# Performance work log

Measured on AMD Instinct MI355X. Metric: run time of the kernel, lower is better.

## Reference

```python
import jax, jax.numpy as jnp
import numpy as np

B, C, H, W = 4, 256, 64, 64
C8 = C // 8

def setup_inputs() -> dict:
    key = jax.random.key(0)
    ks = jax.random.split(key, 9)
    s_in = 1.0 / np.sqrt(C)
    return {
        "feat1": jax.random.normal(ks[0], (B, C, H, W), jnp.float32),
        "feat2": jax.random.normal(ks[1], (B, C, H, W), jnp.float32),
        # 1x1 conv weights stored as [out_ch, in_ch]
        "Wq": jax.random.normal(ks[2], (C8, C), jnp.float32) * s_in,
        "bq": jax.random.normal(ks[3], (C8,), jnp.float32) * s_in,
        "Wk": jax.random.normal(ks[4], (C8, C), jnp.float32) * s_in,
        "bk": jax.random.normal(ks[5], (C8,), jnp.float32) * s_in,
        "Wv": jax.random.normal(ks[6], (C, C), jnp.float32) * s_in,
        "bv": jax.random.normal(ks[7], (C,), jnp.float32) * s_in,
        "gamma": jax.random.normal(ks[8], (1,), jnp.float32) * 0.1,
    }

def reference(feat1, feat2, Wq, bq, Wk, bk, Wv, bv, gamma):
    b, c, h, w = feat1.shape
    n = h * w
    f1 = feat1.reshape(b, c, n)  # [B,C,N]
    f2 = feat2.reshape(b, c, n)
    # 1x1 convs == per-pixel channel matmuls
    q = jnp.einsum("oc,bcn->bno", Wq, f1) + bq            # [B,N,C8]
    k = jnp.einsum("oc,bcn->bon", Wk, f2) + bk[None, :, None]  # [B,C8,N]
    v = jnp.einsum("oc,bcn->bon", Wv, f2) + bv[None, :, None]  # [B,C,N]
    energy = jnp.einsum("bno,bom->bnm", q, k)             # [B,N,N] (unscaled)
    attn = jax.nn.softmax(energy, axis=-1)
    # out[b,c,m] = sum_n v[b,c,n] * attn[b,m,n]
    out = jnp.einsum("bcn,bmn->bcm", v, attn).reshape(b, c, h, w)
    return gamma * out + feat1
```

## Files before the change

kernel.cpp:

```cpp
#include <hip/hip_runtime.h>
#include <hip/hip_bf16.h>
#include <stdint.h>

typedef __attribute__((ext_vector_type(8))) short bf16x8;
typedef __attribute__((ext_vector_type(4))) short short4v;
typedef __attribute__((ext_vector_type(4))) float f32x4;
typedef __attribute__((ext_vector_type(16))) float f32x16;
typedef __attribute__((ext_vector_type(4))) unsigned uint4v;

#define LDS3(p) ((__attribute__((address_space(3))) void*)(p))
#define GLB1(p) ((const __attribute__((address_space(1))) void*)(p))

constexpr int Bc = 4;
constexpr int Cc = 256;
constexpr int Nn = 4096;
constexpr int Dq = 32;
constexpr float L2E = 1.4426950408889634f;

__device__ __forceinline__ short f2b(float x) {
  union { float f; uint32_t u; } v; v.f = x;
  uint32_t r = (v.u + 0x7fffu + ((v.u >> 16) & 1u)) >> 16;
  return (short)(r & 0xffffu);
}
__device__ __forceinline__ float b2f(short s) {
  union { uint32_t u; float f; } v; v.u = ((uint32_t)(uint16_t)s) << 16;
  return v.f;
}
__device__ __forceinline__ unsigned fb(float x) {
  union { float f; unsigned u; } v; v.f = x; return v.u;
}

__global__ __launch_bounds__(256) void prep_transpose(
    const float* __restrict__ f1, const float* __restrict__ f2,
    short* __restrict__ f1T, short* __restrict__ f2T) {
  __shared__ float tile[64][65];
  const int bx = blockIdx.x;
  const int which = bx >> 10;
  const int rem = bx & 1023;
  const int b = rem >> 8;
  const int cb = (rem >> 6) & 3;
  const int nb = rem & 63;
  const float* src = which ? f2 : f1;
  short* dst = which ? f2T : f1T;
  const int c0 = cb * 64, n0 = nb * 64;
  const int tid = threadIdx.x;
  const int lane = tid & 63;
  const int row4 = tid >> 6;
#pragma unroll
  for (int i = 0; i < 16; ++i) {
    const int cl = row4 + i * 4;
    tile[cl][lane] = src[(size_t)(b * Cc + c0 + cl) * Nn + n0 + lane];
  }
  __syncthreads();
#pragma unroll
  for (int i = 0; i < 16; ++i) {
    const int nl = row4 + i * 4;
    dst[(size_t)(b * Nn + n0 + nl) * Cc + c0 + lane] = f2b(tile[lane][nl]);
  }
}

__global__ __launch_bounds__(256) void prep_weights(
    const float* __restrict__ Wq, const float* __restrict__ Wk,
    const float* __restrict__ Wv, short* __restrict__ Wq_b,
    short* __restrict__ Wk_b, short* __restrict__ Wv_b) {
  const int base = (blockIdx.x * 256 + threadIdx.x) * 4;
#pragma unroll
  for (int j = 0; j < 4; ++j) {
    const int idx = base + j;
    if (idx < 8192) Wq_b[idx] = f2b(Wq[idx]);
    else if (idx < 16384) Wk_b[idx - 8192] = f2b(Wk[idx - 8192]);
    else if (idx < 16384 + 65536) Wv_b[idx - 16384] = f2b(Wv[idx - 16384]);
  }
}

__global__ __launch_bounds__(256) void proj_qkv(
    const short* __restrict__ f1T, const short* __restrict__ f2T,
    const short* __restrict__ Wq_b, const float* __restrict__ bq,
    const short* __restrict__ Wk_b, const float* __restrict__ bk,
    const short* __restrict__ Wv_b, const float* __restrict__ bv,
    short* __restrict__ q_ws, short* __restrict__ k_ws,
    short* __restrict__ v_ws) {
  const int bx = blockIdx.x;
  const int b = bx >> 6;
  const int n0 = (bx & 63) * 64;
  const int tid = threadIdx.x;
  const int w = tid >> 6;
  const int lane = tid & 63;
  const int l16 = lane & 15;
  const int g = lane >> 4;

#pragma unroll
  for (int qk = 0; qk < 2; ++qk) {
    const short* X = qk ? f2T : f1T;
    const short* Wm = qk ? Wk_b : Wq_b;
    const float* bias_p = qk ? bk : bq;
    short* outp = qk ? k_ws : q_ws;
    f32x4 accq[2] = {(f32x4){0.f, 0.f, 0.f, 0.f}, (f32x4){0.f, 0.f, 0.f, 0.f}};
#pragma unroll
    for (int kc = 0; kc < 8; ++kc) {
      const bf16x8 a = *(const bf16x8*)&X[(size_t)(b * Nn + n0 + w * 16 + l16) * Cc + kc * 32 + g * 8];
#pragma unroll
      for (int ob = 0; ob < 2; ++ob) {
        const bf16x8 bb = *(const bf16x8*)&Wm[(ob * 16 + l16) * Cc + kc * 32 + g * 8];
        accq[ob] = __builtin_amdgcn_mfma_f32_16x16x32_bf16(a, bb, accq[ob], 0, 0, 0);
      }
    }
#pragma unroll
    for (int ob = 0; ob < 2; ++ob) {
      const float bias = bias_p[ob * 16 + l16];
#pragma unroll
      for (int r = 0; r < 4; ++r) {
        const int n = n0 + w * 16 + g * 4 + r;
        outp[(size_t)(b * Nn + n) * Dq + ob * 16 + l16] = f2b(accq[ob][r] + bias);
      }
    }
  }

  {
    f32x4 acc[4][4];
#pragma unroll
    for (int ci = 0; ci < 4; ++ci)
#pragma unroll
      for (int nb = 0; nb < 4; ++nb) acc[ci][nb] = (f32x4){0.f, 0.f, 0.f, 0.f};
#pragma unroll
    for (int kc = 0; kc < 8; ++kc) {
      bf16x8 bfr[4];
#pragma unroll
      for (int nb = 0; nb < 4; ++nb)
        bfr[nb] = *(const bf16x8*)&f2T[(size_t)(b * Nn + n0 + nb * 16 + l16) * Cc + kc * 32 + g * 8];
#pragma unroll
      for (int ci = 0; ci < 4; ++ci) {
        const bf16x8 afr = *(const bf16x8*)&Wv_b[((w * 4 + ci) * 16 + l16) * Cc + kc * 32 + g * 8];
#pragma unroll
        for (int nb = 0; nb < 4; ++nb)
          acc[ci][nb] = __builtin_amdgcn_mfma_f32_16x16x32_bf16(afr, bfr[nb], acc[ci][nb], 0, 0, 0);
      }
    }
#pragma unroll
    for (int ci = 0; ci < 4; ++ci) {
#pragma unroll
      for (int r = 0; r < 4; ++r) {
        const int c = (w * 4 + ci) * 16 + g * 4 + r;
        const float bias = bv[c];
#pragma unroll
        for (int nb = 0; nb < 4; ++nb) {
          const int n = n0 + nb * 16 + l16;
          v_ws[(size_t)(b * Cc + c) * Nn + n] = f2b(acc[ci][nb][r] + bias);
        }
      }
    }
  }
}

constexpr int NT = 32;
constexpr int VBUF = 256 * NT * 2;
constexpr int SBYTES = 2 * VBUF;

template <int KS>
__global__ __launch_bounds__(256, 2) void attn_kernel(
    const short* __restrict__ q_ws, const short* __restrict__ k_ws,
    const short* __restrict__ v_ws, short* __restrict__ Opart,
    float* __restrict__ mlm, short* __restrict__ mll) {
  constexpr int KSPAN = Nn / KS;
  constexpr int NTILES = KSPAN / NT;
  __shared__ __align__(16) char smem[SBYTES];
  const int bx = blockIdx.x;
  const int swz = (bx & 7) * (16 * KS) + (bx >> 3);
  const int ks = swz >> 7;
  const int rem = swz & 127;
  const int b = rem >> 5;
  const int m0 = (rem & 31) * 128;
  const int n0 = ks * KSPAN;
  const int tid = threadIdx.x;
  const int w = tid >> 6;
  const int lane = tid & 63;
  const int l31 = lane & 31;
  const int h = lane >> 5;

  const short* qbase = q_ws + (size_t)(b * Nn + m0 + w * 32 + l31) * Dq + h * 8;
  const bf16x8 qf0 = *(const bf16x8*)(qbase);
  const bf16x8 qf1 = *(const bf16x8*)(qbase + 16);

  const int kswap = (l31 & 0x13) | ((l31 & 4) << 1) | ((l31 & 8) >> 1);
  const short* kptr = k_ws + (size_t)(b * Nn + n0 + kswap) * Dq + h * 8;

  const int cth = tid >> 2;
  const int koff = 8 * ((tid & 3) ^ (cth & 3));
  const short* vsrc[4];
#pragma unroll
  for (int j = 0; j < 4; ++j)
    vsrc[j] = v_ws + (size_t)(b * Cc + j * 64 + cth) * Nn + n0 + koff;

  f32x16 acc[8] = {};
  float mrun = -INFINITY, lrun = 0.f;

#pragma unroll
  for (int j = 0; j < 4; ++j) {
    char* ldst = &smem[(j * 256 + tid) * 16];
    __builtin_amdgcn_global_load_lds(GLB1(vsrc[j]), LDS3(ldst), 16, 0, 0);
    vsrc[j] += NT;
  }
  bf16x8 kfa = *(const bf16x8*)(kptr);
  bf16x8 kfb = *(const bf16x8*)(kptr + 16);
  kptr += NT * Dq;
  asm volatile("s_waitcnt vmcnt(0)" ::: "memory");
  __syncthreads();

  const f32x16 Z = {};
  unsigned puC[8], puN[8];

  {
    f32x16 sa = __builtin_amdgcn_mfma_f32_32x32x16_bf16(kfa, qf0, Z, 0, 0, 0);
    sa = __builtin_amdgcn_mfma_f32_32x32x16_bf16(kfb, qf1, sa, 0, 0, 0);
    kfa = *(const bf16x8*)(kptr);
    kfb = *(const bf16x8*)(kptr + 16);
    kptr += NT * Dq;
    float t8[8], t4[4];
#pragma unroll
    for (int i = 0; i < 8; ++i) t8[i] = fmaxf(sa[i], sa[i + 8]);
#pragma unroll
    for (int i = 0; i < 4; ++i) t4[i] = fmaxf(t8[i], t8[i + 4]);
    float tmax = fmaxf(fmaxf(t4[0], t4[2]), fmaxf(t4[1], t4[3]));
    tmax = fmaxf(tmax, __shfl_xor(tmax, 32));
    mrun = tmax;
    const float nml = -mrun * L2E;
    float p[16];
#pragma unroll
    for (int r = 0; r < 16; ++r) p[r] = exp2f(fmaf(sa[r], L2E, nml));
#pragma unroll
    for (int q = 0; q < 8; ++q)
      puC[q] = __builtin_amdgcn_perm(fb(p[2 * q + 1]), fb(p[2 * q]), 0x07060302u);
    float s8[8], s4[4];
#pragma unroll
    for (int i = 0; i < 8; ++i) s8[i] = p[i] + p[i + 8];
#pragma unroll
    for (int i = 0; i < 4; ++i) s4[i] = s8[i] + s8[i + 4];
    float psum = (s4[0] + s4[2]) + (s4[1] + s4[3]);
    psum += __shfl_xor(psum, 32);
    lrun = psum;
  }
#pragma unroll
  for (int j = 0; j < 4; ++j) {
    char* ldst = &smem[VBUF + (j * 256 + tid) * 16];
    __builtin_amdgcn_global_load_lds(GLB1(vsrc[j]), LDS3(ldst), 16, 0, 0);
    vsrc[j] += NT;
  }

#pragma unroll 2
  for (int t = 0; t < NTILES; ++t) {
    const int buf = t & 1;
    bool resc = false;
    float sv[16];
    if (t + 1 < NTILES) {
      f32x16 sa = __builtin_amdgcn_mfma_f32_32x32x16_bf16(kfa, qf0, Z, 0, 0, 0);
      sa = __builtin_amdgcn_mfma_f32_32x32x16_bf16(kfb, qf1, sa, 0, 0, 0);
      if (t + 2 < NTILES) {
        kfa = *(const bf16x8*)(kptr);
        kfb = *(const bf16x8*)(kptr + 16);
        kptr += NT * Dq;
      }
      float t8[8], t4[4];
#pragma unroll
      for (int i = 0; i < 8; ++i) t8[i] = fmaxf(sa[i], sa[i + 8]);
#pragma unroll
      for (int i = 0; i < 4; ++i) t4[i] = fmaxf(t8[i], t8[i + 4]);
      float tmax = fmaxf(fmaxf(t4[0], t4[2]), fmaxf(t4[1], t4[3]));
      tmax = fmaxf(tmax, __shfl_xor(tmax, 32));
      resc = __any(tmax > mrun + 8.f);
      if (resc) {
        const float mnew = fmaxf(mrun, tmax);
        const float scl = exp2f((mrun - mnew) * L2E);
#pragma unroll
        for (int r = 0; r < 16; ++r)
          sv[r] = __shfl(scl, (r & 3) + 8 * (r >> 2) + 4 * h);
        lrun *= scl;
        mrun = mnew;
      }
      const float nml = -mrun * L2E;
      float p[16];
#pragma unroll
      for (int r = 0; r < 16; ++r) p[r] = exp2f(fmaf(sa[r], L2E, nml));
#pragma unroll
      for (int q = 0; q < 8; ++q)
        puN[q] = __builtin_amdgcn_perm(fb(p[2 * q + 1]), fb(p[2 * q]), 0x07060302u);
      float s8[8], s4[4];
#pragma unroll
      for (int i = 0; i < 8; ++i) s8[i] = p[i] + p[i + 8];
#pragma unroll
      for (int i = 0; i < 4; ++i) s4[i] = s8[i] + s8[i + 4];
      float psum = (s4[0] + s4[2]) + (s4[1] + s4[3]);
      psum += __shfl_xor(psum, 32);
      lrun += psum;
    }

    __builtin_amdgcn_s_setprio(1);
    const int sb = buf * VBUF;
#pragma unroll
    for (int f = 0; f < 2; ++f) {
      const uint4v au = {puC[4 * f], puC[4 * f + 1], puC[4 * f + 2], puC[4 * f + 3]};
      const bf16x8 A = __builtin_bit_cast(bf16x8, au);
      const char* vbase =
          &smem[sb + l31 * 64 + ((((f << 1) + h) ^ (l31 & 3)) << 4)];
#pragma unroll
      for (int cb = 0; cb < 8; ++cb) {
        const bf16x8 vB = *(const bf16x8*)(vbase + cb * 2048);
        acc[cb] = __builtin_amdgcn_mfma_f32_32x32x16_bf16(A, vB, acc[cb], 0, 0, 0);
      }
    }
    __builtin_amdgcn_s_setprio(0);

    if (t + 1 < NTILES) {
      if (resc) {
#pragma unroll
        for (int cb = 0; cb < 8; ++cb)
#pragma unroll
          for (int r = 0; r < 16; ++r) acc[cb][r] *= sv[r];
      }
      asm volatile("s_waitcnt vmcnt(0)" ::: "memory");
      __syncthreads();
      if (t + 2 < NTILES) {
#pragma unroll
        for (int j = 0; j < 4; ++j) {
          char* ldst = &smem[buf * VBUF + (j * 256 + tid) * 16];
          __builtin_amdgcn_global_load_lds(GLB1(vsrc[j]), LDS3(ldst), 16, 0, 0);
          vsrc[j] += NT;
        }
      }
#pragma unroll
      for (int q = 0; q < 8; ++q) puC[q] = puN[q];
    }
  }

  __syncthreads();
  if (h == 0) {
    const int m = m0 + w * 32 + l31;
    mlm[(size_t)(ks * Bc + b) * Nn + m] = mrun;
    mll[(size_t)(ks * Bc + b) * Nn + m] = f2b(lrun);
  }
  char* strip = smem + w * 5120;
#pragma unroll
  for (int ph = 0; ph < 4; ++ph) {
#pragma unroll
    for (int cb2 = 0; cb2 < 2; ++cb2) {
      const int cb = ph * 2 + cb2;
      const int cs = cb2 * 32 + l31;
#pragma unroll
      for (int q = 0; q < 8; ++q) {
        const int mloc = ((2 * q) & 3) + 8 * (q >> 1) + 4 * h;
        const unsigned pv = __builtin_amdgcn_perm(
            fb(acc[cb][2 * q + 1]), fb(acc[cb][2 * q]), 0x07060302u);
        *(unsigned*)(strip + cs * 80 + mloc * 2) = pv;
      }
    }
    asm volatile("s_waitcnt lgkmcnt(0)" ::: "memory");
#pragma unroll
    for (int i = 0; i < 4; ++i) {
      const int gi = i * 64 + lane;
      const int cs = gi >> 2, gq = gi & 3;
      const uint4v vv = *(const uint4v*)(strip + cs * 80 + gq * 16);
      const int cg = ph * 64 + cs;
      const size_t off =
          ((size_t)(ks * Bc + b) * Cc + cg) * Nn + m0 + w * 32 + gq * 8;
      *(uint4v*)&Opart[off] = vv;
    }
    asm volatile("s_waitcnt lgkmcnt(0)" ::: "memory");
  }
}

template <int KS>
__global__ __launch_bounds__(256) void combine_kernel(
    const short* __restrict__ Opart, const float* __restrict__ mlm,
    const short* __restrict__ mll, const float* __restrict__ feat1,
    const float* __restrict__ gamma_p, float* __restrict__ out) {
  __shared__ float aLDS[KS][64];
  const int bx = blockIdx.x;
  const int b = bx >> 6;
  const int m0 = (bx & 63) * 64;
  const int tid = threadIdx.x;
  if (tid < 64) {
    const int m = m0 + tid;
    float mm[KS], ll[KS], ms = -INFINITY;
#pragma unroll
    for (int ks = 0; ks < KS; ++ks) {
      mm[ks] = mlm[(size_t)(ks * Bc + b) * Nn + m];
      ll[ks] = b2f(mll[(size_t)(ks * Bc + b) * Nn + m]);
      ms = fmaxf(ms, mm[ks]);
    }
    float es[KS], lsum = 0.f;
#pragma unroll
    for (int ks = 0; ks < KS; ++ks) {
      es[ks] = exp2f((mm[ks] - ms) * L2E);
      lsum += ll[ks] * es[ks];
    }
    const float inv = 1.f / lsum;
#pragma unroll
    for (int ks = 0; ks < KS; ++ks) aLDS[ks][tid] = es[ks] * inv;
  }
  __syncthreads();
  const int mg = tid & 7;
  const int cb = tid >> 3;
  float aks[KS][8];
#pragma unroll
  for (int ks = 0; ks < KS; ++ks)
#pragma unroll
    for (int j = 0; j < 8; ++j) aks[ks][j] = aLDS[ks][mg * 8 + j];
  const float gam = gamma_p[0];
#pragma unroll 2
  for (int i = 0; i < 8; ++i) {
    const int c = cb + i * 32;
    float v[8] = {0.f, 0.f, 0.f, 0.f, 0.f, 0.f, 0.f, 0.f};
#pragma unroll
    for (int ks = 0; ks < KS; ++ks) {
      const bf16x8 ov = *(const bf16x8*)
          &Opart[((size_t)(ks * Bc + b) * Cc + c) * Nn + m0 + mg * 8];
#pragma unroll
      for (int j = 0; j < 8; ++j) v[j] += b2f(ov[j]) * aks[ks][j];
    }
    const size_t base = ((size_t)(b * Cc + c)) * Nn + m0 + mg * 8;
    const f32x4 fa = *(const f32x4*)&feat1[base];
    const f32x4 fbv = *(const f32x4*)&feat1[base + 4];
    f32x4 o0, o1;
#pragma unroll
    for (int j = 0; j < 4; ++j) {
      o0[j] = gam * v[j] + fa[j];
      o1[j] = gam * v[4 + j] + fbv[j];
    }
    *(f32x4*)&out[base] = o0;
    *(f32x4*)&out[base + 4] = o1;
  }
}

extern "C" void kernel_launch(void* const* d_in, const int* in_sizes, int n_in,
                              void* d_out, int out_size, void* d_ws,
                              size_t ws_size, hipStream_t stream) {
  const float* feat1 = (const float*)d_in[0];
  const float* feat2 = (const float*)d_in[1];
  const float* Wq = (const float*)d_in[2];
  const float* bq = (const float*)d_in[3];
  const float* Wk = (const float*)d_in[4];
  const float* bk = (const float*)d_in[5];
  const float* Wv = (const float*)d_in[6];
  const float* bv = (const float*)d_in[7];
  const float* gamma = (const float*)d_in[8];
  float* out = (float*)d_out;
  char* ws = (char*)d_ws;

  const size_t need4 = 44433408;
  if (ws_size >= need4) {
    short* Opart = (short*)(ws + 0);
    short* f1T  = (short*)(ws + 0);
    short* f2T  = (short*)(ws + 8388608);
    short* Wq_b = (short*)(ws + 16777216);
    short* Wk_b = (short*)(ws + 16793600);
    short* Wv_b = (short*)(ws + 16809984);
    short* q_ws = (short*)(ws + 33554432);
    short* k_ws = (short*)(ws + 34603008);
    short* v_ws = (short*)(ws + 35651584);
    float* mlm  = (float*)(ws + 44040192);
    short* mll  = (short*)(ws + 44302336);

    prep_transpose<<<2048, 256, 0, stream>>>(feat1, feat2, f1T, f2T);
    prep_weights<<<80, 256, 0, stream>>>(Wq, Wk, Wv, Wq_b, Wk_b, Wv_b);
    proj_qkv<<<256, 256, 0, stream>>>(f1T, f2T, Wq_b, bq, Wk_b, bk, Wv_b, bv,
                                      q_ws, k_ws, v_ws);
    attn_kernel<4><<<512, 256, 0, stream>>>(q_ws, k_ws, v_ws, Opart, mlm, mll);
    combine_kernel<4><<<256, 256, 0, stream>>>(Opart, mlm, mll, feat1, gamma,
                                               out);
  } else {
    short* Opart = (short*)(ws + 0);
    short* f1T  = (short*)(ws + 0);
    short* f2T  = (short*)(ws + 8388608);
    short* Wq_b = (short*)(ws + 16777216);
    short* Wk_b = (short*)(ws + 16793600);
    short* Wv_b = (short*)(ws + 16809984);
    short* q_ws = (short*)(ws + 16941056);
    short* k_ws = (short*)(ws + 17989632);
    short* v_ws = (short*)(ws + 19038208);
    float* mlm  = (float*)(ws + 27426816);
    short* mll  = (short*)(ws + 27557888);

    prep_transpose<<<2048, 256, 0, stream>>>(feat1, feat2, f1T, f2T);
    prep_weights<<<80, 256, 0, stream>>>(Wq, Wk, Wv, Wq_b, Wk_b, Wv_b);
    proj_qkv<<<256, 256, 0, stream>>>(f1T, f2T, Wq_b, bq, Wk_b, bk, Wv_b, bv,
                                      q_ws, k_ws, v_ws);
    attn_kernel<2><<<256, 256, 0, stream>>>(q_ws, k_ws, v_ws, Opart, mlm, mll);
    combine_kernel<2><<<256, 256, 0, stream>>>(Opart, mlm, mll, feat1, gamma,
                                               out);
  }
}
```

Before: 112.3 us.

## Fuse transpose into projection kernel and double attention V tile size

Removes the separate prep_transpose kernel: the projection kernel now loads fp32 feature tiles, transposes and converts them to bf16 in shared memory, and runs the Q/K/V MFMAs from LDS. This avoids writing and re-reading the transposed bf16 copies in global memory and saves one launch. The attention kernel's V tile grows from 32 to 64 keys with two score sub-steps per iteration, halving barriers and global-to-LDS load rounds, at the cost of twice the LDS per block (which may lower occupancy) and a longer, more complex loop body.

```diff
diff --git a/kernel.cpp b/kernel.cpp
--- a/kernel.cpp
+++ b/kernel.cpp
@@ -30,35 +30,6 @@
   union { float f; unsigned u; } v; v.f = x; return v.u;
 }
 
-__global__ __launch_bounds__(256) void prep_transpose(
-    const float* __restrict__ f1, const float* __restrict__ f2,
-    short* __restrict__ f1T, short* __restrict__ f2T) {
-  __shared__ float tile[64][65];
-  const int bx = blockIdx.x;
-  const int which = bx >> 10;
-  const int rem = bx & 1023;
-  const int b = rem >> 8;
-  const int cb = (rem >> 6) & 3;
-  const int nb = rem & 63;
-  const float* src = which ? f2 : f1;
-  short* dst = which ? f2T : f1T;
-  const int c0 = cb * 64, n0 = nb * 64;
-  const int tid = threadIdx.x;
-  const int lane = tid & 63;
-  const int row4 = tid >> 6;
-#pragma unroll
-  for (int i = 0; i < 16; ++i) {
-    const int cl = row4 + i * 4;
-    tile[cl][lane] = src[(size_t)(b * Cc + c0 + cl) * Nn + n0 + lane];
-  }
-  __syncthreads();
-#pragma unroll
-  for (int i = 0; i < 16; ++i) {
-    const int nl = row4 + i * 4;
-    dst[(size_t)(b * Nn + n0 + nl) * Cc + c0 + lane] = f2b(tile[lane][nl]);
-  }
-}
-
 __global__ __launch_bounds__(256) void prep_weights(
     const float* __restrict__ Wq, const float* __restrict__ Wk,
     const float* __restrict__ Wv, short* __restrict__ Wq_b,
@@ -73,13 +44,15 @@
   }
 }
 
-__global__ __launch_bounds__(256) void proj_qkv(
-    const short* __restrict__ f1T, const short* __restrict__ f2T,
+__global__ __launch_bounds__(256) void proj_fused(
+    const float* __restrict__ f1, const float* __restrict__ f2,
     const short* __restrict__ Wq_b, const float* __restrict__ bq,
     const short* __restrict__ Wk_b, const float* __restrict__ bk,
     const short* __restrict__ Wv_b, const float* __restrict__ bv,
     short* __restrict__ q_ws, short* __restrict__ k_ws,
     short* __restrict__ v_ws) {
+  __shared__ float ftile[64][65];
+  __shared__ short T[64][264];
   const int bx = blockIdx.x;
   const int b = bx >> 6;
   const int n0 = (bx & 63) * 64;
@@ -88,17 +61,36 @@
   const int lane = tid & 63;
   const int l16 = lane & 15;
   const int g = lane >> 4;
-
-#pragma unroll
-  for (int qk = 0; qk < 2; ++qk) {
-    const short* X = qk ? f2T : f1T;
-    const short* Wm = qk ? Wk_b : Wq_b;
-    const float* bias_p = qk ? bk : bq;
-    short* outp = qk ? k_ws : q_ws;
+  const int lane64 = tid & 63;
+  const int row4 = tid >> 6;
+
+  auto build = [&](const float* __restrict__ src) {
+#pragma unroll
+    for (int cc = 0; cc < 4; ++cc) {
+      __syncthreads();
+#pragma unroll
+      for (int i = 0; i < 16; ++i) {
+        const int cl = row4 + i * 4;
+        ftile[cl][lane64] =
+            src[(size_t)(b * Cc + cc * 64 + cl) * Nn + n0 + lane64];
+      }
+      __syncthreads();
+#pragma unroll
+      for (int i = 0; i < 16; ++i) {
+        const int nl = row4 + i * 4;
+        T[nl][cc * 64 + lane64] = f2b(ftile[lane64][nl]);
+      }
+    }
+    __syncthreads();
+  };
+
+  auto qk_phase = [&](const short* __restrict__ Wm,
+                      const float* __restrict__ bias_p,
+                      short* __restrict__ outp) {
     f32x4 accq[2] = {(f32x4){0.f, 0.f, 0.f, 0.f}, (f32x4){0.f, 0.f, 0.f, 0.f}};
 #pragma unroll
     for (int kc = 0; kc < 8; ++kc) {
-      const bf16x8 a = *(const bf16x8*)&X[(size_t)(b * Nn + n0 + w * 16 + l16) * Cc + kc * 32 + g * 8];
+      const bf16x8 a = *(const bf16x8*)&T[w * 16 + l16][kc * 32 + g * 8];
 #pragma unroll
       for (int ob = 0; ob < 2; ++ob) {
         const bf16x8 bb = *(const bf16x8*)&Wm[(ob * 16 + l16) * Cc + kc * 32 + g * 8];
@@ -114,8 +106,14 @@
         outp[(size_t)(b * Nn + n) * Dq + ob * 16 + l16] = f2b(accq[ob][r] + bias);
       }
     }
-  }
-
+  };
+
+  build(f1);
+  qk_phase(Wq_b, bq, q_ws);
+  __syncthreads();
+
+  build(f2);
+  qk_phase(Wk_b, bk, k_ws);
   {
     f32x4 acc[4][4];
 #pragma unroll
@@ -127,7 +125,7 @@
       bf16x8 bfr[4];
 #pragma unroll
       for (int nb = 0; nb < 4; ++nb)
-        bfr[nb] = *(const bf16x8*)&f2T[(size_t)(b * Nn + n0 + nb * 16 + l16) * Cc + kc * 32 + g * 8];
+        bfr[nb] = *(const bf16x8*)&T[nb * 16 + l16][kc * 32 + g * 8];
 #pragma unroll
       for (int ci = 0; ci < 4; ++ci) {
         const bf16x8 afr = *(const bf16x8*)&Wv_b[((w * 4 + ci) * 16 + l16) * Cc + kc * 32 + g * 8];
@@ -152,7 +150,7 @@
   }
 }
 
-constexpr int NT = 32;
+constexpr int NT = 64;
 constexpr int VBUF = 256 * NT * 2;
 constexpr int SBYTES = 2 * VBUF;
 
@@ -184,37 +182,37 @@
   const int kswap = (l31 & 0x13) | ((l31 & 4) << 1) | ((l31 & 8) >> 1);
   const short* kptr = k_ws + (size_t)(b * Nn + n0 + kswap) * Dq + h * 8;
 
-  const int cth = tid >> 2;
-  const int koff = 8 * ((tid & 3) ^ (cth & 3));
-  const short* vsrc[4];
-#pragma unroll
-  for (int j = 0; j < 4; ++j)
-    vsrc[j] = v_ws + (size_t)(b * Cc + j * 64 + cth) * Nn + n0 + koff;
+  const int cth = tid >> 3;
+  const int c7 = cth & 7;
+  const int koff = 8 * ((tid & 7) ^ c7);
+  const short* vsrc[8];
+#pragma unroll
+  for (int j = 0; j < 8; ++j)
+    vsrc[j] = v_ws + (size_t)(b * Cc + j * 32 + cth) * Nn + n0 + koff;
 
   f32x16 acc[8] = {};
   float mrun = -INFINITY, lrun = 0.f;
 
 #pragma unroll
-  for (int j = 0; j < 4; ++j) {
+  for (int j = 0; j < 8; ++j) {
     char* ldst = &smem[(j * 256 + tid) * 16];
     __builtin_amdgcn_global_load_lds(GLB1(vsrc[j]), LDS3(ldst), 16, 0, 0);
     vsrc[j] += NT;
   }
   bf16x8 kfa = *(const bf16x8*)(kptr);
   bf16x8 kfb = *(const bf16x8*)(kptr + 16);
-  kptr += NT * Dq;
+  kptr += 32 * Dq;
   asm volatile("s_waitcnt vmcnt(0)" ::: "memory");
   __syncthreads();
 
   const f32x16 Z = {};
-  unsigned puC[8], puN[8];
-
+  unsigned puA[8], puB[8];
   {
     f32x16 sa = __builtin_amdgcn_mfma_f32_32x32x16_bf16(kfa, qf0, Z, 0, 0, 0);
     sa = __builtin_amdgcn_mfma_f32_32x32x16_bf16(kfb, qf1, sa, 0, 0, 0);
     kfa = *(const bf16x8*)(kptr);
     kfb = *(const bf16x8*)(kptr + 16);
-    kptr += NT * Dq;
+    kptr += 32 * Dq;
     float t8[8], t4[4];
 #pragma unroll
     for (int i = 0; i < 8; ++i) t8[i] = fmaxf(sa[i], sa[i + 8]);
@@ -229,7 +227,7 @@
     for (int r = 0; r < 16; ++r) p[r] = exp2f(fmaf(sa[r], L2E, nml));
 #pragma unroll
     for (int q = 0; q < 8; ++q)
-      puC[q] = __builtin_amdgcn_perm(fb(p[2 * q + 1]), fb(p[2 * q]), 0x07060302u);
+      puA[q] = __builtin_amdgcn_perm(fb(p[2 * q + 1]), fb(p[2 * q]), 0x07060302u);
     float s8[8], s4[4];
 #pragma unroll
     for (int i = 0; i < 8; ++i) s8[i] = p[i] + p[i + 8];
@@ -240,49 +238,69 @@
     lrun = psum;
   }
 #pragma unroll
-  for (int j = 0; j < 4; ++j) {
+  for (int j = 0; j < 8; ++j) {
     char* ldst = &smem[VBUF + (j * 256 + tid) * 16];
     __builtin_amdgcn_global_load_lds(GLB1(vsrc[j]), LDS3(ldst), 16, 0, 0);
     vsrc[j] += NT;
   }
 
-#pragma unroll 2
   for (int t = 0; t < NTILES; ++t) {
-    const int buf = t & 1;
-    bool resc = false;
-    float sv[16];
-    if (t + 1 < NTILES) {
-      f32x16 sa = __builtin_amdgcn_mfma_f32_32x32x16_bf16(kfa, qf0, Z, 0, 0, 0);
-      sa = __builtin_amdgcn_mfma_f32_32x32x16_bf16(kfb, qf1, sa, 0, 0, 0);
-      if (t + 2 < NTILES) {
-        kfa = *(const bf16x8*)(kptr);
-        kfb = *(const bf16x8*)(kptr + 16);
-        kptr += NT * Dq;
-      }
-      float t8[8], t4[4];
-#pragma unroll
-      for (int i = 0; i < 8; ++i) t8[i] = fmaxf(sa[i], sa[i + 8]);
-#pragma unroll
-      for (int i = 0; i < 4; ++i) t4[i] = fmaxf(t8[i], t8[i + 4]);
-      float tmax = fmaxf(fmaxf(t4[0], t4[2]), fmaxf(t4[1], t4[3]));
-      tmax = fmaxf(tmax, __shfl_xor(tmax, 32));
-      resc = __any(tmax > mrun + 8.f);
-      if (resc) {
-        const float mnew = fmaxf(mrun, tmax);
-        const float scl = exp2f((mrun - mnew) * L2E);
-#pragma unroll
-        for (int r = 0; r < 16; ++r)
-          sv[r] = __shfl(scl, (r & 3) + 8 * (r >> 2) + 4 * h);
-        lrun *= scl;
-        mrun = mnew;
-      }
+    const int sb = (t & 1) * VBUF;
+    const bool have2 = (t + 1 < NTILES);
+
+    f32x16 sa = __builtin_amdgcn_mfma_f32_32x32x16_bf16(kfa, qf0, Z, 0, 0, 0);
+    sa = __builtin_amdgcn_mfma_f32_32x32x16_bf16(kfb, qf1, sa, 0, 0, 0);
+    if (have2) {
+      kfa = *(const bf16x8*)(kptr);
+      kfb = *(const bf16x8*)(kptr + 16);
+      kptr += 32 * Dq;
+    }
+    float t8[8], t4[4];
+#pragma unroll
+    for (int i = 0; i < 8; ++i) t8[i] = fmaxf(sa[i], sa[i + 8]);
+#pragma unroll
+    for (int i = 0; i < 4; ++i) t4[i] = fmaxf(t8[i], t8[i + 4]);
+    float tmax = fmaxf(fmaxf(t4[0], t4[2]), fmaxf(t4[1], t4[3]));
+    tmax = fmaxf(tmax, __shfl_xor(tmax, 32));
+    const bool resc = __any(tmax > mrun + 8.f);
+
+    __builtin_amdgcn_s_setprio(1);
+#pragma unroll
+    for (int fl = 0; fl < 2; ++fl) {
+      const uint4v au = {puA[4 * fl], puA[4 * fl + 1], puA[4 * fl + 2], puA[4 * fl + 3]};
+      const bf16x8 A = __builtin_bit_cast(bf16x8, au);
+      const int sg = 2 * fl + h;
+      const char* vbase = &smem[sb + l31 * 128 + ((sg ^ (l31 & 7)) << 4)];
+#pragma unroll
+      for (int cb = 0; cb < 8; ++cb) {
+        const bf16x8 vB = *(const bf16x8*)(vbase + cb * 4096);
+        acc[cb] = __builtin_amdgcn_mfma_f32_32x32x16_bf16(A, vB, acc[cb], 0, 0, 0);
+      }
+    }
+    __builtin_amdgcn_s_setprio(0);
+
+    if (resc) {
+      const float mnew = fmaxf(mrun, tmax);
+      const float scl = exp2f((mrun - mnew) * L2E);
+      float sv[16];
+#pragma unroll
+      for (int r = 0; r < 16; ++r)
+        sv[r] = __shfl(scl, (r & 3) + 8 * (r >> 2) + 4 * h);
+#pragma unroll
+      for (int cb = 0; cb < 8; ++cb)
+#pragma unroll
+        for (int r = 0; r < 16; ++r) acc[cb][r] *= sv[r];
+      lrun *= scl;
+      mrun = mnew;
+    }
+    {
       const float nml = -mrun * L2E;
       float p[16];
 #pragma unroll
       for (int r = 0; r < 16; ++r) p[r] = exp2f(fmaf(sa[r], L2E, nml));
 #pragma unroll
       for (int q = 0; q < 8; ++q)
-        puN[q] = __builtin_amdgcn_perm(fb(p[2 * q + 1]), fb(p[2 * q]), 0x07060302u);
+        puB[q] = __builtin_amdgcn_perm(fb(p[2 * q + 1]), fb(p[2 * q]), 0x07060302u);
       float s8[8], s4[4];
 #pragma unroll
       for (int i = 0; i < 8; ++i) s8[i] = p[i] + p[i + 8];
@@ -293,41 +311,82 @@
       lrun += psum;
     }
 
+    f32x16 sa2 = Z;
+    float tmax2 = 0.f;
+    bool resc2 = false;
+    if (have2) {
+      sa2 = __builtin_amdgcn_mfma_f32_32x32x16_bf16(kfa, qf0, Z, 0, 0, 0);
+      sa2 = __builtin_amdgcn_mfma_f32_32x32x16_bf16(kfb, qf1, sa2, 0, 0, 0);
+      kfa = *(const bf16x8*)(kptr);
+      kfb = *(const bf16x8*)(kptr + 16);
+      kptr += 32 * Dq;
+      float u8[8], u4[4];
+#pragma unroll
+      for (int i = 0; i < 8; ++i) u8[i] = fmaxf(sa2[i], sa2[i + 8]);
+#pragma unroll
+      for (int i = 0; i < 4; ++i) u4[i] = fmaxf(u8[i], u8[i + 4]);
+      tmax2 = fmaxf(fmaxf(u4[0], u4[2]), fmaxf(u4[1], u4[3]));
+      tmax2 = fmaxf(tmax2, __shfl_xor(tmax2, 32));
+      resc2 = __any(tmax2 > mrun + 8.f);
+    }
+
     __builtin_amdgcn_s_setprio(1);
-    const int sb = buf * VBUF;
-#pragma unroll
-    for (int f = 0; f < 2; ++f) {
-      const uint4v au = {puC[4 * f], puC[4 * f + 1], puC[4 * f + 2], puC[4 * f + 3]};
+#pragma unroll
+    for (int fl = 0; fl < 2; ++fl) {
+      const uint4v au = {puB[4 * fl], puB[4 * fl + 1], puB[4 * fl + 2], puB[4 * fl + 3]};
       const bf16x8 A = __builtin_bit_cast(bf16x8, au);
-      const char* vbase =
-          &smem[sb + l31 * 64 + ((((f << 1) + h) ^ (l31 & 3)) << 4)];
+      const int sg = 4 + 2 * fl + h;
+      const char* vbase = &smem[sb + l31 * 128 + ((sg ^ (l31 & 7)) << 4)];
 #pragma unroll
       for (int cb = 0; cb < 8; ++cb) {
-        const bf16x8 vB = *(const bf16x8*)(vbase + cb * 2048);
+        const bf16x8 vB = *(const bf16x8*)(vbase + cb * 4096);
         acc[cb] = __builtin_amdgcn_mfma_f32_32x32x16_bf16(A, vB, acc[cb], 0, 0, 0);
       }
     }
     __builtin_amdgcn_s_setprio(0);
 
-    if (t + 1 < NTILES) {
-      if (resc) {
+    if (have2) {
+      if (resc2) {
+        const float mnew = fmaxf(mrun, tmax2);
+        const float scl = exp2f((mrun - mnew) * L2E);
+        float sv[16];
+#pragma unroll
+        for (int r = 0; r < 16; ++r)
+          sv[r] = __shfl(scl, (r & 3) + 8 * (r >> 2) + 4 * h);
 #pragma unroll
         for (int cb = 0; cb < 8; ++cb)
 #pragma unroll
           for (int r = 0; r < 16; ++r) acc[cb][r] *= sv[r];
+        lrun *= scl;
+        mrun = mnew;
+      }
+      {
+        const float nml = -mrun * L2E;
+        float p[16];
+#pragma unroll
+        for (int r = 0; r < 16; ++r) p[r] = exp2f(fmaf(sa2[r], L2E, nml));
+#pragma unroll
+        for (int q = 0; q < 8; ++q)
+          puA[q] = __builtin_amdgcn_perm(fb(p[2 * q + 1]), fb(p[2 * q]), 0x07060302u);
+        float s8[8], s4[4];
+#pragma unroll
+        for (int i = 0; i < 8; ++i) s8[i] = p[i] + p[i + 8];
+#pragma unroll
+        for (int i = 0; i < 4; ++i) s4[i] = s8[i] + s8[i + 4];
+        float psum = (s4[0] + s4[2]) + (s4[1] + s4[3]);
+        psum += __shfl_xor(psum, 32);
+        lrun += psum;
       }
       asm volatile("s_waitcnt vmcnt(0)" ::: "memory");
       __syncthreads();
       if (t + 2 < NTILES) {
 #pragma unroll
-        for (int j = 0; j < 4; ++j) {
-          char* ldst = &smem[buf * VBUF + (j * 256 + tid) * 16];
+        for (int j = 0; j < 8; ++j) {
+          char* ldst = &smem[sb + (j * 256 + tid) * 16];
           __builtin_amdgcn_global_load_lds(GLB1(vsrc[j]), LDS3(ldst), 16, 0, 0);
           vsrc[j] += NT;
         }
       }
-#pragma unroll
-      for (int q = 0; q < 8; ++q) puC[q] = puN[q];
     }
   }
 
@@ -337,12 +396,12 @@
     mlm[(size_t)(ks * Bc + b) * Nn + m] = mrun;
     mll[(size_t)(ks * Bc + b) * Nn + m] = f2b(lrun);
   }
-  char* strip = smem + w * 5120;
-#pragma unroll
-  for (int ph = 0; ph < 4; ++ph) {
-#pragma unroll
-    for (int cb2 = 0; cb2 < 2; ++cb2) {
-      const int cb = ph * 2 + cb2;
+  char* strip = smem + w * 10240;
+#pragma unroll
+  for (int ph = 0; ph < 2; ++ph) {
+#pragma unroll
+    for (int cb2 = 0; cb2 < 4; ++cb2) {
+      const int cb = ph * 4 + cb2;
       const int cs = cb2 * 32 + l31;
 #pragma unroll
       for (int q = 0; q < 8; ++q) {
@@ -354,11 +413,11 @@
     }
     asm volatile("s_waitcnt lgkmcnt(0)" ::: "memory");
 #pragma unroll
-    for (int i = 0; i < 4; ++i) {
+    for (int i = 0; i < 8; ++i) {
       const int gi = i * 64 + lane;
       const int cs = gi >> 2, gq = gi & 3;
       const uint4v vv = *(const uint4v*)(strip + cs * 80 + gq * 16);
-      const int cg = ph * 64 + cs;
+      const int cg = ph * 128 + cs;
       const size_t off =
           ((size_t)(ks * Bc + b) * Cc + cg) * Nn + m0 + w * 32 + gq * 8;
       *(uint4v*)&Opart[off] = vv;
@@ -448,8 +507,6 @@
   const size_t need4 = 44433408;
   if (ws_size >= need4) {
     short* Opart = (short*)(ws + 0);
-    short* f1T  = (short*)(ws + 0);
-    short* f2T  = (short*)(ws + 8388608);
     short* Wq_b = (short*)(ws + 16777216);
     short* Wk_b = (short*)(ws + 16793600);
     short* Wv_b = (short*)(ws + 16809984);
@@ -459,17 +516,14 @@
     float* mlm  = (float*)(ws + 44040192);
     short* mll  = (short*)(ws + 44302336);
 
-    prep_transpose<<<2048, 256, 0, stream>>>(feat1, feat2, f1T, f2T);
     prep_weights<<<80, 256, 0, stream>>>(Wq, Wk, Wv, Wq_b, Wk_b, Wv_b);
-    proj_qkv<<<256, 256, 0, stream>>>(f1T, f2T, Wq_b, bq, Wk_b, bk, Wv_b, bv,
-                                      q_ws, k_ws, v_ws);
+    proj_fused<<<256, 256, 0, stream>>>(feat1, feat2, Wq_b, bq, Wk_b, bk,
+                                        Wv_b, bv, q_ws, k_ws, v_ws);
     attn_kernel<4><<<512, 256, 0, stream>>>(q_ws, k_ws, v_ws, Opart, mlm, mll);
     combine_kernel<4><<<256, 256, 0, stream>>>(Opart, mlm, mll, feat1, gamma,
                                                out);
   } else {
     short* Opart = (short*)(ws + 0);
-    short* f1T  = (short*)(ws + 0);
-    short* f2T  = (short*)(ws + 8388608);
     short* Wq_b = (short*)(ws + 16777216);
     short* Wk_b = (short*)(ws + 16793600);
     short* Wv_b = (short*)(ws + 16809984);
@@ -479,10 +533,9 @@
     float* mlm  = (float*)(ws + 27426816);
     short* mll  = (short*)(ws + 27557888);
 
-    prep_transpose<<<2048, 256, 0, stream>>>(feat1, feat2, f1T, f2T);
     prep_weights<<<80, 256, 0, stream>>>(Wq, Wk, Wv, Wq_b, Wk_b, Wv_b);
-    proj_qkv<<<256, 256, 0, stream>>>(f1T, f2T, Wq_b, bq, Wk_b, bk, Wv_b, bv,
-                                      q_ws, k_ws, v_ws);
+    proj_fused<<<256, 256, 0, stream>>>(feat1, feat2, Wq_b, bq, Wk_b, bk,
+                                        Wv_b, bv, q_ws, k_ws, v_ws);
     attn_kernel<2><<<256, 256, 0, stream>>>(q_ws, k_ws, v_ws, Opart, mlm, mll);
     combine_kernel<2><<<256, 256, 0, stream>>>(Opart, mlm, mll, feat1, gamma,
                                                out);
```

After: 98.78 us. -12.0%, faster.
